# Kernel optimization log

Measured on AMD Instinct MI355X. Metric: run time of the kernel, lower is better.

The kernel has to match this reference:

```python
import jax, jax.numpy as jnp
import numpy as np

N = 4096
DIN, DOUT, HID, CUTS = 16, 16, 16, 8
RADIUS = 9.0
SCALES = (1.0, 2.0, 3.0, 5.0, 10.0)
REG = 0.01
CHUNK = 512
GROUPS = 4
DINF = DIN + 2 * len(SCALES)  # 26


def leaky(v):
    return jnp.where(v >= 0, v, 0.2 * v)


def sqdist(a, b):
    d2 = jnp.sum(a * a, -1)[:, None] + jnp.sum(b * b, -1)[None, :] - 2.0 * (a @ b.T)
    return jnp.maximum(d2, 0.0)


def tangent_vectors(n):
    # Duff et al. branchless orthonormal basis, as in dMaSIF geometry_processing
    x, y, z = n[..., 0], n[..., 1], n[..., 2]
    s = jnp.where(z >= 0, 1.0, -1.0)
    a = -1.0 / (s + z)
    b = x * y * a
    t1 = jnp.stack([1.0 + s * x * x * a, s * b, -s * x], -1)
    t2 = jnp.stack([b, s + y * y * a, -y], -1)
    return jnp.stack([t1, t2], axis=-2)  # (..., 2, 3)


def group_norm(x, w, b, eps=1e-5):
    # torch GroupNorm(4, C) applied on (1, C, N): normalize over (C/G, N) per group
    n, c = x.shape
    xt = x.T.reshape(GROUPS, c // GROUPS, n)
    m = jnp.mean(xt, axis=(1, 2), keepdims=True)
    v = jnp.mean((xt - m) ** 2, axis=(1, 2), keepdims=True)
    xt = (xt - m) / jnp.sqrt(v + eps)
    return (xt.reshape(c, n) * w[:, None] + b[:, None]).T


def curvature_features(verts, normals):
    # dMaSIF curvatures(): per-scale Gaussian-window covariances, shape operator S = PPt^-1 PQt
    # Pairwise sums factorized into matmuls with the (N,N) window (no (N,N,8) intermediates).
    n_pts = verts.shape[0]
    d2 = sqdist(verts, verts)
    xx = (verts[:, :, None] * verts[:, None, :]).reshape(n_pts, 9)
    feats = []
    for s in SCALES:
        w = jnp.exp(-d2 / (2.0 * s * s))
        u_n = w @ normals  # scale-smoothed normals
        ns = u_n / jnp.maximum(jnp.linalg.norm(u_n, axis=-1, keepdims=True), 1e-12)
        uv = tangent_vectors(ns)  # (N,2,3)
        s0 = jnp.sum(w, 1)
        sx = w @ verts
        sn = w @ ns
        sxx = (w @ xx).reshape(n_pts, 3, 3)
        xn = (verts[:, :, None] * ns[:, None, :]).reshape(n_pts, 9)
        sxn = (w @ xn).reshape(n_pts, 3, 3)
        # sum_j w_ij (x_j-x_i)(x_j-x_i)^T  and  sum_j w_ij (x_j-x_i)(n_j-n_i)^T
        cxx = sxx - verts[:, :, None] * sx[:, None, :] - sx[:, :, None] * verts[:, None, :] \
              + s0[:, None, None] * verts[:, :, None] * verts[:, None, :]
        cxn = sxn - verts[:, :, None] * sn[:, None, :] - sx[:, :, None] * ns[:, None, :] \
              + s0[:, None, None] * verts[:, :, None] * ns[:, None, :]
        ppt = jnp.einsum('nka,nab,nlb->nkl', uv, cxx, uv) + REG * jnp.eye(2, dtype=verts.dtype)
        pqt = jnp.einsum('nka,nab,nlb->nkl', uv, cxn, uv)
        S = jnp.linalg.solve(ppt, pqt)  # (N,2,2)
        feats.append(jnp.clip(S[:, 0, 0] + S[:, 1, 1], -1.0, 1.0))            # mean curvature
        feats.append(jnp.clip(S[:, 0, 0] * S[:, 1, 1] - S[:, 0, 1] * S[:, 1, 0], -1.0, 1.0))  # gauss
    return jnp.stack(feats, -1)  # (N, 2*len(SCALES))


def _forward(verts, vnormals, x, os_w1, os_b1, os_w2, os_b2,
             ni_w1, ni_b1, ni_w2, ni_b2, gn_in_w, gn_in_b,
             cv_a1, cv_b1, cv_a2, cv_b2, no_w1, no_b1, no_w2, no_b2,
             gn_out_w, gn_out_b, ll_w1, ll_b1, ll_w2, ll_b2, lt_w, lt_b):
    curv = curvature_features(verts, vnormals)
    xf = jnp.concatenate([x, curv], axis=-1)  # (N, DINF)
    w = leaky(xf @ os_w1.T + os_b1) @ os_w2.T + os_b2  # orientation scores (N,1)

    # --- load_mesh: steer tangent frames along the gradient of w ---
    p = verts / RADIUS
    ndot = vnormals @ vnormals.T
    W = jnp.exp(-sqdist(p, p) * (2.0 - ndot) ** 2)  # pseudo-geodesic Gaussian window
    uv = tangent_vectors(vnormals)  # (N,2,3)
    ov3 = W @ (w * p) - (W @ w) * p  # sum_j W_ij w_j (x_j - x_i), factorized
    ov = jnp.einsum('nkd,nd->nk', uv, ov3) + 1e-5
    u = ov / jnp.sqrt(jnp.sum(ov * ov, -1, keepdims=True))
    ex, ey = u[:, 0:1], u[:, 1:2]
    u0, v0 = uv[:, 0], uv[:, 1]
    nuv = jnp.concatenate([vnormals[:, None, :],
                           (ex * u0 + ey * v0)[:, None, :],
                           (-ey * u0 + ex * v0)[:, None, :]], axis=1)  # (N,3,3)

    # --- dMaSIFConv layer ---
    h = leaky(leaky(xf @ ni_w1.T + ni_b1) @ ni_w2.T + ni_b2)
    h = group_norm(h, gn_in_w, gn_in_b)  # (N, HID)
    n_all = nuv[:, 0]
    nc = N // CHUNK
    pc = p.reshape(nc, CHUNK, 3)
    nuvc = nuv.reshape(nc, CHUNK, 3, 3)

    def block(args):
        pi, nuvi = args  # (C,3), (C,3,3)
        dx = p[None, :, :] - pi[:, None, :]  # (C,N,3)
        d2 = jnp.sum(dx * dx, -1)
        win = jnp.exp(-d2 * (2.0 - nuvi[:, 0] @ n_all.T) ** 2)  # (C,N)
        X = jnp.einsum('ckd,cnd->cnk', nuvi, dx)  # local coords (C,N,3)
        y = jax.nn.relu(X @ cv_a1.T + cv_b1) @ cv_a2.T + cv_b2  # filter MLP (C,N,HID)
        return jnp.einsum('cn,cnh,nh->ch', win, y, h)

    xi = jax.lax.map(jax.checkpoint(block), (pc, nuvc)).reshape(N, HID)
    xi = group_norm(leaky(leaky(xi @ no_w1.T + no_b1) @ no_w2.T + no_b2), gn_out_w, gn_out_b)
    xi = jax.nn.relu(xi @ ll_w1.T + ll_b1) @ ll_w2.T + ll_b2  # linear_layers[0]
    return xf @ lt_w.T + lt_b + xi  # linear_transform skip + conv branch


def setup_inputs():
    key = jax.random.key(0)
    ks = jax.random.split(key, 20)

    def lin(k, o, i):
        wk = jax.random.fold_in(k, 0)
        bk = jax.random.fold_in(k, 1)
        return ((1.0 / np.sqrt(i)) * jax.random.normal(wk, (o, i)),
                0.01 * jax.random.normal(bk, (o,)))

    verts = 10.0 * jax.random.normal(ks[0], (N, 3))
    vn = jax.random.normal(ks[1], (N, 3))
    vnormals = vn / jnp.linalg.norm(vn, axis=-1, keepdims=True)
    x = jax.random.normal(ks[2], (N, DIN))
    os_w1, os_b1 = lin(ks[3], DOUT, DINF)
    os_w2, os_b2 = lin(ks[4], 1, DOUT)
    ni_w1, ni_b1 = lin(ks[5], HID, DINF)
    ni_w2, ni_b2 = lin(ks[6], HID, HID)
    cv_a1 = jax.random.normal(ks[7], (CUTS, 3))
    cv_b1 = jax.random.uniform(ks[8], (CUTS,)) * 0.8 * jnp.sqrt(jnp.sum(cv_a1 ** 2, -1))
    cv_a2 = jax.random.uniform(ks[9], (HID, CUTS), minval=-1.0, maxval=1.0) / np.sqrt(CUTS)
    cv_b2 = jax.random.normal(ks[10], (HID,)) * 0.5 * jnp.sqrt(jnp.sum(cv_a2 ** 2, -1))
    no_w1, no_b1 = lin(ks[11], DOUT, HID)
    no_w2, no_b2 = lin(ks[12], DOUT, DOUT)
    ll_w1, ll_b1 = lin(ks[13], DOUT, DOUT)
    ll_w2, ll_b2 = lin(ks[14], DOUT, DOUT)
    lt_w, lt_b = lin(ks[15], DOUT, DINF)
    return {'verts': verts, 'vnormals': vnormals, 'x': x,
            'os_w1': os_w1, 'os_b1': os_b1, 'os_w2': os_w2, 'os_b2': os_b2,
            'ni_w1': ni_w1, 'ni_b1': ni_b1, 'ni_w2': ni_w2, 'ni_b2': ni_b2,
            'gn_in_w': jnp.ones(HID), 'gn_in_b': jnp.zeros(HID),
            'cv_a1': cv_a1, 'cv_b1': cv_b1, 'cv_a2': cv_a2, 'cv_b2': cv_b2,
            'no_w1': no_w1, 'no_b1': no_b1, 'no_w2': no_w2, 'no_b2': no_b2,
            'gn_out_w': jnp.ones(DOUT), 'gn_out_b': jnp.zeros(DOUT),
            'll_w1': ll_w1, 'll_b1': ll_b1, 'll_w2': ll_w2, 'll_b2': ll_b2,
            'lt_w': lt_w, 'lt_b': lt_b}


def reference(verts, vnormals, x, os_w1, os_b1, os_w2, os_b2,
              ni_w1, ni_b1, ni_w2, ni_b2, gn_in_w, gn_in_b,
              cv_a1, cv_b1, cv_a2, cv_b2, no_w1, no_b1, no_w2, no_b2,
              gn_out_w, gn_out_b, ll_w1, ll_b1, ll_w2, ll_b2, lt_w, lt_b):
    return _forward(verts, vnormals, x, os_w1, os_b1, os_w2, os_b2,
                    ni_w1, ni_b1, ni_w2, ni_b2, gn_in_w, gn_in_b,
                    cv_a1, cv_b1, cv_a2, cv_b2, no_w1, no_b1, no_w2, no_b2,
                    gn_out_w, gn_out_b, ll_w1, ll_b1, ll_w2, ll_b2, lt_w, lt_b)
```

## Files before the change

kernel.cpp:

```cpp
#include <hip/hip_runtime.h>
#include <hip/hip_bf16.h>
#include <math.h>

#define NPTS 4096
#define DINF 26
#define LOG2E 1.44269504088896f
#define JSPL 4

typedef float f32x4v __attribute__((ext_vector_type(4)));
typedef __bf16 bf16x8v __attribute__((ext_vector_type(8)));
typedef unsigned short ushort_t;

__device__ __forceinline__ float ldb(const float* p, int i){ return p[i]; }
__device__ __forceinline__ float lk(float v){ return v >= 0.0f ? v : 0.2f*v; }
__device__ __forceinline__ float wsum64(float v){
#pragma unroll
  for(int o=32;o>0;o>>=1) v += __shfl_down(v,o);
  return v;
}
__device__ __forceinline__ unsigned short f2bf(float f){
  return __builtin_bit_cast(unsigned short, __float2bfloat16(f));
}
__device__ __forceinline__ float bf2f(unsigned short u){
  return __bfloat162float(__builtin_bit_cast(__hip_bfloat16, u));
}
__device__ __forceinline__ void wave_lds_fence(){
  __builtin_amdgcn_wave_barrier();
  __builtin_amdgcn_s_waitcnt(0xC07F);
  __builtin_amdgcn_wave_barrier();
}
__device__ __forceinline__ void tangent(float nx,float ny,float nz,float* t1,float* t2){
  float s = (nz >= 0.0f) ? 1.0f : -1.0f;
  float a = -1.0f/(s+nz);
  float b = nx*ny*a;
  t1[0]=1.0f+s*nx*nx*a; t1[1]=s*b; t1[2]=-s*nx;
  t2[0]=b; t2[1]=s+ny*ny*a; t2[2]=-ny;
}

__global__ __launch_bounds__(256) void k0_convert(const float* __restrict__ verts,
                                                  const float* __restrict__ vnorm,
                                                  const float* __restrict__ x,
                                                  float* __restrict__ vertsF,
                                                  float* __restrict__ nF,
                                                  float* __restrict__ pF,
                                                  float* __restrict__ xfF){
  int i = blockIdx.x*blockDim.x + threadIdx.x;
  if(i >= NPTS) return;
#pragma unroll
  for(int d=0;d<3;d++){
    float v = verts[i*3+d];
    vertsF[i*3+d]=v;
    pF[i*3+d]=v*(1.0f/9.0f);
    nF[i*3+d]=vnorm[i*3+d];
  }
#pragma unroll
  for(int c=0;c<16;c++) xfF[i*DINF+c]=x[i*16+c];
}

__global__ __launch_bounds__(256) void kF(const float* __restrict__ vertsF,
                                          const float* __restrict__ nF,
                                          ushort_t* __restrict__ F1h,
                                          ushort_t* __restrict__ F1l){
  int j = blockIdx.x*256 + threadIdx.x;
  float vx=vertsF[j*3+0], vy=vertsF[j*3+1], vz=vertsF[j*3+2];
  float fv[16];
  fv[0]=1.0f; fv[1]=vx; fv[2]=vy; fv[3]=vz;
  fv[4]=vx*vx; fv[5]=vx*vy; fv[6]=vx*vz; fv[7]=vy*vy; fv[8]=vy*vz; fv[9]=vz*vz;
  fv[10]=nF[j*3+0]; fv[11]=nF[j*3+1]; fv[12]=nF[j*3+2];
  fv[13]=0.0f; fv[14]=0.0f; fv[15]=0.0f;
#pragma unroll
  for(int c=0;c<16;c++){
    unsigned short h=f2bf(fv[c]);
    F1h[c*NPTS+j]=h;
    F1l[c*NPTS+j]=f2bf(fv[c]-bf2f(h));
  }
}

__global__ __launch_bounds__(256) void k1m(const float* __restrict__ vertsF,
                                           const ushort_t* __restrict__ F1h,
                                           const ushort_t* __restrict__ F1l,
                                           float* __restrict__ sc){
  __shared__ __align__(16) float vq[4][64][4];
  __shared__ float red[4][16][16];
  const float c2e[5] = {0.5f*LOG2E, 0.125f*LOG2E, (1.0f/18.0f)*LOG2E,
                        0.02f*LOG2E, 0.005f*LOG2E};
  int lane = threadIdx.x & 63, w = threadIdx.x >> 6;
  int c16 = lane & 15, q = lane >> 4;
  int it = blockIdx.x >> 2, jseg = blockIdx.x & (JSPL-1);
  int i0 = it*16;
  int ia = i0 + c16;
  float vix=vertsF[ia*3+0], viy=vertsF[ia*3+1], viz=vertsF[ia*3+2];
  float nsqi = vix*vix+viy*viy+viz*viz;
  f32x4v acc[5];
#pragma unroll
  for(int s=0;s<5;s++) acc[s] = (f32x4v){0.0f,0.0f,0.0f,0.0f};

  int jbeg = jseg*(NPTS/JSPL) + w*(NPTS/JSPL/4);
  int jend = jbeg + (NPTS/JSPL/4);
#pragma unroll 1
  for(int jb=jbeg; jb<jend; jb+=64){
    int j = jb + lane;
    float vx=vertsF[j*3+0], vy=vertsF[j*3+1], vz=vertsF[j*3+2];
    *(float4*)&vq[w][lane][0] = make_float4(vx,vy,vz,vx*vx+vy*vy+vz*vz);
    wave_lds_fence();
#pragma unroll
    for(int q2=0;q2<2;q2++){
      int rb = q2*32 + q*8;
      bf16x8v bh = *(const bf16x8v*)(F1h + c16*NPTS + jb + rb);
      bf16x8v bl = *(const bf16x8v*)(F1l + c16*NPTS + jb + rb);
      bf16x8v af[5];
#pragma unroll
      for(int t=0;t<8;t++){
        float4 vv = *(const float4*)&vq[w][rb+t][0];
        float dot = vix*vv.x + viy*vv.y + viz*vv.z;
        float d2 = fmaxf(nsqi + vv.w - 2.0f*dot, 0.0f);
#pragma unroll
        for(int s=0;s<5;s++)
          af[s][t] = __builtin_bit_cast(__bf16, f2bf(exp2f(-d2*c2e[s])));
      }
#pragma unroll
      for(int s=0;s<5;s++){
        acc[s] = __builtin_amdgcn_mfma_f32_16x16x32_bf16(af[s], bh, acc[s], 0,0,0);
        acc[s] = __builtin_amdgcn_mfma_f32_16x16x32_bf16(af[s], bl, acc[s], 0,0,0);
      }
    }
    wave_lds_fence();
  }
#pragma unroll
  for(int s=0;s<5;s++){
#pragma unroll
    for(int r=0;r<4;r++) red[w][q*4+r][c16] = acc[s][r];
    __syncthreads();
    if(w==0){
      float* base = sc + (size_t)s*13*NPTS;
#pragma unroll
      for(int r=0;r<4;r++){
        int m = q*4+r, i = i0+m;
        float D = red[0][m][c16]+red[1][m][c16]+red[2][m][c16]+red[3][m][c16];
        if(c16==0)       atomicAdd(&base[i], D);
        else if(c16<4)   atomicAdd(&base[NPTS + i*3 + (c16-1)], D);
        else if(c16<10)  atomicAdd(&base[4*NPTS + i*6 + (c16-4)], D);
        else if(c16<13)  atomicAdd(&base[10*NPTS + i*3 + (c16-10)], D);
      }
    }
    __syncthreads();
  }
}

__global__ __launch_bounds__(256) void k2p(const float* __restrict__ vertsF,
                                           const float* __restrict__ sc,
                                           ushort_t* __restrict__ F2h,
                                           ushort_t* __restrict__ F2l){
  int idx = blockIdx.x*256 + threadIdx.x;
  int j = idx & (NPTS-1);
  int s = idx >> 12;
  float vx=vertsF[j*3+0], vy=vertsF[j*3+1], vz=vertsF[j*3+2];
  const float* ub = sc + (size_t)s*13*NPTS + 10*NPTS + (size_t)j*3;
  float ux=ub[0], uy=ub[1], uz=ub[2];
  float inv = 1.0f/fmaxf(sqrtf(ux*ux+uy*uy+uz*uz), 1e-12f);
  float n0=ux*inv, n1=uy*inv, n2=uz*inv;
  float fv[16];
  fv[0]=n0; fv[1]=n1; fv[2]=n2;
  fv[3]=vx*n0; fv[4]=vx*n1; fv[5]=vx*n2;
  fv[6]=vy*n0; fv[7]=vy*n1; fv[8]=vy*n2;
  fv[9]=vz*n0; fv[10]=vz*n1; fv[11]=vz*n2;
  fv[12]=0.0f; fv[13]=0.0f; fv[14]=0.0f; fv[15]=0.0f;
#pragma unroll
  for(int c=0;c<16;c++){
    unsigned short h=f2bf(fv[c]);
    F2h[((size_t)s*16+c)*NPTS+j]=h;
    F2l[((size_t)s*16+c)*NPTS+j]=f2bf(fv[c]-bf2f(h));
  }
}

__global__ __launch_bounds__(256) void k2m(const float* __restrict__ vertsF,
                                           const ushort_t* __restrict__ F2h,
                                           const ushort_t* __restrict__ F2l,
                                           float* __restrict__ mom2){
  __shared__ __align__(16) float vq[4][64][4];
  __shared__ float red[4][16][16];
  const float c2e[5] = {0.5f*LOG2E, 0.125f*LOG2E, (1.0f/18.0f)*LOG2E,
                        0.02f*LOG2E, 0.005f*LOG2E};
  int lane = threadIdx.x & 63, w = threadIdx.x >> 6;
  int c16 = lane & 15, q = lane >> 4;
  int it = blockIdx.x >> 2, jseg = blockIdx.x & (JSPL-1);
  int i0 = it*16;
  int ia = i0 + c16;
  float vix=vertsF[ia*3+0], viy=vertsF[ia*3+1], viz=vertsF[ia*3+2];
  float nsqi = vix*vix+viy*viy+viz*viz;
  f32x4v acc[5];
#pragma unroll
  for(int s=0;s<5;s++) acc[s] = (f32x4v){0.0f,0.0f,0.0f,0.0f};

  int jbeg = jseg*(NPTS/JSPL) + w*(NPTS/JSPL/4);
  int jend = jbeg + (NPTS/JSPL/4);
#pragma unroll 1
  for(int jb=jbeg; jb<jend; jb+=64){
    int j = jb + lane;
    float vx=vertsF[j*3+0], vy=vertsF[j*3+1], vz=vertsF[j*3+2];
    *(float4*)&vq[w][lane][0] = make_float4(vx,vy,vz,vx*vx+vy*vy+vz*vz);
    wave_lds_fence();
#pragma unroll
    for(int q2=0;q2<2;q2++){
      int rb = q2*32 + q*8;
      float d2t[8];
#pragma unroll
      for(int t=0;t<8;t++){
        float4 vv = *(const float4*)&vq[w][rb+t][0];
        float dot = vix*vv.x + viy*vv.y + viz*vv.z;
        d2t[t] = fmaxf(nsqi + vv.w - 2.0f*dot, 0.0f);
      }
#pragma unroll
      for(int s=0;s<5;s++){
        bf16x8v bh = *(const bf16x8v*)(F2h + ((size_t)s*16+c16)*NPTS + jb + rb);
        bf16x8v bl = *(const bf16x8v*)(F2l + ((size_t)s*16+c16)*NPTS + jb + rb);
        bf16x8v af;
#pragma unroll
        for(int t=0;t<8;t++)
          af[t] = __builtin_bit_cast(__bf16, f2bf(exp2f(-d2t[t]*c2e[s])));
        acc[s] = __builtin_amdgcn_mfma_f32_16x16x32_bf16(af, bh, acc[s], 0,0,0);
        acc[s] = __builtin_amdgcn_mfma_f32_16x16x32_bf16(af, bl, acc[s], 0,0,0);
      }
    }
    wave_lds_fence();
  }
#pragma unroll
  for(int s=0;s<5;s++){
#pragma unroll
    for(int r=0;r<4;r++) red[w][q*4+r][c16] = acc[s][r];
    __syncthreads();
    if(w==0){
#pragma unroll
      for(int r=0;r<4;r++){
        int m = q*4+r, i = i0+m;
        float D = red[0][m][c16]+red[1][m][c16]+red[2][m][c16]+red[3][m][c16];
        if(c16<12) atomicAdd(&mom2[((size_t)s*NPTS + i)*12 + c16], D);
      }
    }
    __syncthreads();
  }
}

__global__ __launch_bounds__(256) void k2s(const float* __restrict__ vertsF,
                                           const float* __restrict__ sc,
                                           const float* __restrict__ mom2,
                                           float* __restrict__ xfF){
  int idx = blockIdx.x*256 + threadIdx.x;
  int i = idx & (NPTS-1);
  int s = idx >> 12;
  const float* base = sc + (size_t)s*13*NPTS;
  float v[3] = { vertsF[i*3+0], vertsF[i*3+1], vertsF[i*3+2] };
  float s0 = base[i];
  float sx[3] = { base[NPTS+i*3+0], base[NPTS+i*3+1], base[NPTS+i*3+2] };
  float sxx6[6];
#pragma unroll
  for(int k=0;k<6;k++) sxx6[k]=base[4*NPTS+i*6+k];
  float ux=base[10*NPTS+i*3+0], uy=base[10*NPTS+i*3+1], uz=base[10*NPTS+i*3+2];
  float invn = 1.0f/fmaxf(sqrtf(ux*ux+uy*uy+uz*uz), 1e-12f);
  float nsi[3] = { ux*invn, uy*invn, uz*invn };
  const float* M2 = mom2 + ((size_t)s*NPTS + i)*12;
  float sn[3] = { M2[0], M2[1], M2[2] };
  float sxn[3][3];
#pragma unroll
  for(int a=0;a<3;a++)
#pragma unroll
    for(int b=0;b<3;b++) sxn[a][b]=M2[3+a*3+b];
  const int m6[3][3]={{0,1,2},{1,3,4},{2,4,5}};
  float cxx[3][3], cxn[3][3];
#pragma unroll
  for(int a=0;a<3;a++)
#pragma unroll
    for(int b=0;b<3;b++){
      cxx[a][b]=sxx6[m6[a][b]] - v[a]*sx[b] - sx[a]*v[b] + s0*v[a]*v[b];
      cxn[a][b]=sxn[a][b]    - v[a]*sn[b] - sx[a]*nsi[b] + s0*v[a]*nsi[b];
    }
  float t1[3],t2[3];
  tangent(nsi[0],nsi[1],nsi[2],t1,t2);
  float ppt[2][2], pqt[2][2];
#pragma unroll
  for(int k=0;k<2;k++){
    const float* tk = (k==0)?t1:t2;
#pragma unroll
    for(int l=0;l<2;l++){
      const float* tl = (l==0)?t1:t2;
      float accx=0.0f, accn=0.0f;
#pragma unroll
      for(int a=0;a<3;a++)
#pragma unroll
        for(int b=0;b<3;b++){
          accx += tk[a]*cxx[a][b]*tl[b];
          accn += tk[a]*cxn[a][b]*tl[b];
        }
      ppt[k][l]=accx + ((k==l)?0.01f:0.0f);
      pqt[k][l]=accn;
    }
  }
  float det = ppt[0][0]*ppt[1][1]-ppt[0][1]*ppt[1][0];
  float id = 1.0f/det;
  float S00=( ppt[1][1]*pqt[0][0]-ppt[0][1]*pqt[1][0])*id;
  float S01=( ppt[1][1]*pqt[0][1]-ppt[0][1]*pqt[1][1])*id;
  float S10=(-ppt[1][0]*pqt[0][0]+ppt[0][0]*pqt[1][0])*id;
  float S11=(-ppt[1][0]*pqt[0][1]+ppt[0][0]*pqt[1][1])*id;
  float f0=fminf(fmaxf(S00+S11,-1.0f),1.0f);
  float f1=fminf(fmaxf(S00*S11-S01*S10,-1.0f),1.0f);
  xfF[i*DINF+16+2*s]=f0;
  xfF[i*DINF+17+2*s]=f1;
}

__global__ __launch_bounds__(256) void k3_mlps(const float* __restrict__ xfF,
    const float* os_w1, const float* os_b1, const float* os_w2, const float* os_b2,
    const float* ni_w1, const float* ni_b1, const float* ni_w2, const float* ni_b2,
    float* __restrict__ wOS, float* __restrict__ hPre, float* __restrict__ stats){
  int i = blockIdx.x*256 + threadIdx.x;
  int lane = threadIdx.x & 63;
  float xf[DINF];
#pragma unroll
  for(int k=0;k<DINF;k++) xf[k]=xfF[i*DINF+k];
  float h1[16];
#pragma unroll
  for(int o=0;o<16;o++){
    float t=ldb(os_b1,o);
#pragma unroll
    for(int k=0;k<DINF;k++) t += xf[k]*ldb(os_w1,o*DINF+k);
    h1[o]=lk(t);
  }
  float w=ldb(os_b2,0);
#pragma unroll
  for(int o=0;o<16;o++) w += h1[o]*ldb(os_w2,o);
  wOS[i]=w;
#pragma unroll
  for(int o=0;o<16;o++){
    float t=ldb(ni_b1,o);
#pragma unroll
    for(int k=0;k<DINF;k++) t += xf[k]*ldb(ni_w1,o*DINF+k);
    h1[o]=lk(t);
  }
  float h2[16];
#pragma unroll
  for(int o=0;o<16;o++){
    float t=ldb(ni_b2,o);
#pragma unroll
    for(int k=0;k<16;k++) t += h1[k]*ldb(ni_w2,o*16+k);
    h2[o]=lk(t);
    hPre[i*16+o]=h2[o];
  }
  float gs[4]={0,0,0,0}, gq[4]={0,0,0,0};
#pragma unroll
  for(int c=0;c<16;c++){ gs[c>>2]+=h2[c]; gq[c>>2]+=h2[c]*h2[c]; }
  __shared__ float ls[8];
  if(threadIdx.x<8) ls[threadIdx.x]=0.0f;
  __syncthreads();
#pragma unroll
  for(int g=0;g<4;g++){ gs[g]=wsum64(gs[g]); gq[g]=wsum64(gq[g]); }
  if(lane==0){
#pragma unroll
    for(int g=0;g<4;g++){ atomicAdd(&ls[2*g],gs[g]); atomicAdd(&ls[2*g+1],gq[g]); }
  }
  __syncthreads();
  if(threadIdx.x<8) atomicAdd(&stats[threadIdx.x], ls[threadIdx.x]);
}

__global__ __launch_bounds__(256) void k3c_gn(const float* __restrict__ hPre,
                                              const float* __restrict__ stats,
                                              const float* gw, const float* gb,
                                              ushort_t* __restrict__ hTb){
  int i = blockIdx.x*256 + threadIdx.x;
  float m[4], r[4];
#pragma unroll
  for(int g=0;g<4;g++){
    float mean = stats[2*g]*(1.0f/(4.0f*NPTS));
    float var  = stats[2*g+1]*(1.0f/(4.0f*NPTS)) - mean*mean;
    m[g]=mean; r[g]=1.0f/sqrtf(var+1e-5f);
  }
#pragma unroll
  for(int c=0;c<16;c++){
    int g=c>>2;
    float v=(hPre[i*16+c]-m[g])*r[g]*ldb(gw,c)+ldb(gb,c);
    hTb[c*NPTS+i]=f2bf(v);
  }
}

__global__ __launch_bounds__(256) void kB(const float* __restrict__ pF,
                                          const float* __restrict__ wOS,
                                          ushort_t* __restrict__ B4h,
                                          ushort_t* __restrict__ B4l){
  int j = blockIdx.x*256 + threadIdx.x;
  float wj=wOS[j];
  float fv[16];
  fv[0]=wj*pF[j*3+0]; fv[1]=wj*pF[j*3+1]; fv[2]=wj*pF[j*3+2]; fv[3]=wj;
#pragma unroll
  for(int c=4;c<16;c++) fv[c]=0.0f;
#pragma unroll
  for(int c=0;c<16;c++){
    unsigned short h=f2bf(fv[c]);
    B4h[c*NPTS+j]=h;
    B4l[c*NPTS+j]=f2bf(fv[c]-bf2f(h));
  }
}

__global__ __launch_bounds__(512) void k4m(const float* __restrict__ pF,
                                           const float* __restrict__ nF,
                                           const ushort_t* __restrict__ B4h,
                                           const ushort_t* __restrict__ B4l,
                                           float* __restrict__ nuvF){
  __shared__ __align__(16) float vq[8][64][8];
  __shared__ float red[8][16][4];
  int lane = threadIdx.x & 63, w = threadIdx.x >> 6;
  int c16 = lane & 15, q = lane >> 4;
  int i0 = blockIdx.x*16;
  int ia = i0 + c16;
  float pix=pF[ia*3+0], piy=pF[ia*3+1], piz=pF[ia*3+2];
  float nix=nF[ia*3+0], niy=nF[ia*3+1], niz=nF[ia*3+2];
  f32x4v acc = {0.0f,0.0f,0.0f,0.0f};

#pragma unroll 1
  for(int jb=w*512; jb<w*512+512; jb+=64){
    int j = jb + lane;
    *(float4*)&vq[w][lane][0] = make_float4(pF[j*3+0],pF[j*3+1],pF[j*3+2],0.0f);
    *(float4*)&vq[w][lane][4] = make_float4(nF[j*3+0],nF[j*3+1],nF[j*3+2],0.0f);
    wave_lds_fence();
#pragma unroll
    for(int q2=0;q2<2;q2++){
      int rb = q2*32 + q*8;
      bf16x8v bh = *(const bf16x8v*)(B4h + c16*NPTS + jb + rb);
      bf16x8v bl = *(const bf16x8v*)(B4l + c16*NPTS + jb + rb);
      bf16x8v af;
#pragma unroll
      for(int t=0;t<8;t++){
        float4 P  = *(const float4*)&vq[w][rb+t][0];
        float4 Nj = *(const float4*)&vq[w][rb+t][4];
        float dx=P.x-pix, dy=P.y-piy, dz=P.z-piz;
        float d2=dx*dx+dy*dy+dz*dz;
        float f=2.0f-(Nj.x*nix+Nj.y*niy+Nj.z*niz);
        af[t]=__builtin_bit_cast(__bf16, f2bf(exp2f(-d2*f*f*LOG2E)));
      }
      acc = __builtin_amdgcn_mfma_f32_16x16x32_bf16(af, bh, acc, 0,0,0);
      acc = __builtin_amdgcn_mfma_f32_16x16x32_bf16(af, bl, acc, 0,0,0);
    }
    wave_lds_fence();
  }
#pragma unroll
  for(int r=0;r<4;r++) if(c16<4) red[w][q*4+r][c16]=acc[r];
  __syncthreads();
  if(threadIdx.x<16){
    int tid=threadIdx.x, i=i0+tid;
    float a0=0,a1=0,a2=0,a3=0;
#pragma unroll
    for(int ww=0;ww<8;ww++){
      a0+=red[ww][tid][0]; a1+=red[ww][tid][1];
      a2+=red[ww][tid][2]; a3+=red[ww][tid][3];
    }
    float pix2=pF[i*3+0], piy2=pF[i*3+1], piz2=pF[i*3+2];
    float nix2=nF[i*3+0], niy2=nF[i*3+1], niz2=nF[i*3+2];
    float o0=a0-a3*pix2, o1=a1-a3*piy2, o2=a2-a3*piz2;
    float t1[3],t2[3];
    tangent(nix2,niy2,niz2,t1,t2);
    float ov0=t1[0]*o0+t1[1]*o1+t1[2]*o2+1e-5f;
    float ov1=t2[0]*o0+t2[1]*o1+t2[2]*o2+1e-5f;
    float inv=1.0f/sqrtf(ov0*ov0+ov1*ov1);
    float ex=ov0*inv, ey=ov1*inv;
    nuvF[i*9+0]=nix2; nuvF[i*9+1]=niy2; nuvF[i*9+2]=niz2;
    nuvF[i*9+3]= ex*t1[0]+ey*t2[0]; nuvF[i*9+4]= ex*t1[1]+ey*t2[1]; nuvF[i*9+5]= ex*t1[2]+ey*t2[2];
    nuvF[i*9+6]=-ey*t1[0]+ex*t2[0]; nuvF[i*9+7]=-ey*t1[1]+ex*t2[1]; nuvF[i*9+8]=-ey*t1[2]+ex*t2[2];
  }
}

__global__ __launch_bounds__(256) void k5_conv(const float* __restrict__ pF,
                                               const float* __restrict__ nF,
                                               const float* __restrict__ nuvF,
                                               const ushort_t* __restrict__ hTb,
                                               const float* cv_a1, const float* cv_b1,
                                               const float* cv_a2, const float* cv_b2,
                                               float* __restrict__ xiP){
  __shared__ __align__(16) float vq[4][64][8];
  __shared__ float red[4][64][4];
  int lane = threadIdx.x & 63, w = threadIdx.x >> 6;
  int c16 = lane & 15, q = lane >> 4;
  int it = blockIdx.x >> 2, jseg = blockIdx.x & (JSPL-1);
  int i0 = it*16;
  int i = i0 + c16;
  float pix=pF[i*3+0], piy=pF[i*3+1], piz=pF[i*3+2];
  float nu[9];
#pragma unroll
  for(int k=0;k<9;k++) nu[k]=nuvF[i*9+k];
  float a1w[8][3], b1w[8];
#pragma unroll
  for(int c=0;c<8;c++){
    a1w[c][0]=cv_a1[c*3+0]; a1w[c][1]=cv_a1[c*3+1]; a1w[c][2]=cv_a1[c*3+2];
    b1w[c]=cv_b1[c];
  }
  f32x4v acc[9];
#pragma unroll
  for(int c=0;c<9;c++) acc[c]=(f32x4v){0.0f,0.0f,0.0f,0.0f};

  int jbeg = jseg*(NPTS/JSPL) + w*(NPTS/JSPL/4);
  int jend = jbeg + (NPTS/JSPL/4);
#pragma unroll 1
  for(int jb=jbeg; jb<jend; jb+=64){
    int j = jb + lane;
    *(float4*)&vq[w][lane][0] = make_float4(pF[j*3+0],pF[j*3+1],pF[j*3+2],0.0f);
    *(float4*)&vq[w][lane][4] = make_float4(nF[j*3+0],nF[j*3+1],nF[j*3+2],0.0f);
    wave_lds_fence();
#pragma unroll
    for(int q2=0;q2<2;q2++){
      int jb2 = jb + q2*32;
      bf16x8v bfr = *(const bf16x8v*)(hTb + c16*NPTS + jb2 + q*8);
      bf16x8v af[9];
#pragma unroll
      for(int t=0;t<8;t++){
        int rloc = q2*32 + q*8 + t;
        float4 P  = *(const float4*)&vq[w][rloc][0];
        float4 Nj = *(const float4*)&vq[w][rloc][4];
        float dx=P.x-pix, dy=P.y-piy, dz=P.z-piz;
        float d2=dx*dx+dy*dy+dz*dz;
        float f=2.0f-(Nj.x*nu[0]+Nj.y*nu[1]+Nj.z*nu[2]);
        float win=exp2f(-d2*f*f*LOG2E);
        float X0=nu[0]*dx+nu[1]*dy+nu[2]*dz;
        float X1=nu[3]*dx+nu[4]*dy+nu[5]*dz;
        float X2=nu[6]*dx+nu[7]*dy+nu[8]*dz;
#pragma unroll
        for(int c=0;c<8;c++){
          float r=fmaf(X0,a1w[c][0],fmaf(X1,a1w[c][1],fmaf(X2,a1w[c][2],b1w[c])));
          af[c][t]=__builtin_bit_cast(__bf16, f2bf(win*fmaxf(r,0.0f)));
        }
        af[8][t]=__builtin_bit_cast(__bf16, f2bf(win));
      }
#pragma unroll
      for(int c=0;c<9;c++)
        acc[c] = __builtin_amdgcn_mfma_f32_16x16x32_bf16(af[c], bfr, acc[c], 0,0,0);
    }
    wave_lds_fence();
  }
  float a2row[8];
#pragma unroll
  for(int c=0;c<8;c++) a2row[c]=cv_a2[c16*8+c];
  float b2v = cv_b2[c16];
#pragma unroll
  for(int r=0;r<4;r++){
    float xi = acc[8][r]*b2v;
#pragma unroll
    for(int c=0;c<8;c++) xi += acc[c][r]*a2row[c];
    red[w][lane][r]=xi;
  }
  __syncthreads();
  if(w==0){
#pragma unroll
    for(int r=0;r<4;r++){
      float v = red[0][lane][r]+red[1][lane][r]+red[2][lane][r]+red[3][lane][r];
      xiP[((size_t)jseg*NPTS + (i0 + q*4 + r))*16 + c16] = v;
    }
  }
}

__global__ __launch_bounds__(256) void k6a(const float* __restrict__ xiP,
    const float* no_w1, const float* no_b1, const float* no_w2, const float* no_b2,
    float* __restrict__ tF, float* __restrict__ stats2){
  int i = blockIdx.x*256 + threadIdx.x;
  int lane = threadIdx.x & 63;
  float xi[16];
#pragma unroll
  for(int k=0;k<16;k++){
    float v=0.0f;
#pragma unroll
    for(int s=0;s<JSPL;s++) v += xiP[((size_t)s*NPTS + i)*16 + k];
    xi[k]=v;
  }
  float t1[16];
#pragma unroll
  for(int o=0;o<16;o++){
    float t=ldb(no_b1,o);
#pragma unroll
    for(int k=0;k<16;k++) t += xi[k]*ldb(no_w1,o*16+k);
    t1[o]=lk(t);
  }
  float t2[16];
#pragma unroll
  for(int o=0;o<16;o++){
    float t=ldb(no_b2,o);
#pragma unroll
    for(int k=0;k<16;k++) t += t1[k]*ldb(no_w2,o*16+k);
    t2[o]=lk(t);
    tF[i*16+o]=t2[o];
  }
  float gs[4]={0,0,0,0}, gq[4]={0,0,0,0};
#pragma unroll
  for(int c=0;c<16;c++){ gs[c>>2]+=t2[c]; gq[c>>2]+=t2[c]*t2[c]; }
  __shared__ float ls[8];
  if(threadIdx.x<8) ls[threadIdx.x]=0.0f;
  __syncthreads();
#pragma unroll
  for(int g=0;g<4;g++){ gs[g]=wsum64(gs[g]); gq[g]=wsum64(gq[g]); }
  if(lane==0){
#pragma unroll
    for(int g=0;g<4;g++){ atomicAdd(&ls[2*g],gs[g]); atomicAdd(&ls[2*g+1],gq[g]); }
  }
  __syncthreads();
  if(threadIdx.x<8) atomicAdd(&stats2[threadIdx.x], ls[threadIdx.x]);
}

__global__ __launch_bounds__(256) void k6c(const float* __restrict__ tF,
    const float* __restrict__ xfF, const float* __restrict__ stats2,
    const float* gw, const float* gb,
    const float* ll_w1, const float* ll_b1, const float* ll_w2, const float* ll_b2,
    const float* lt_w, const float* lt_b,
    float* __restrict__ out){
  int i = blockIdx.x*256 + threadIdx.x;
  float m[4], r[4];
#pragma unroll
  for(int g=0;g<4;g++){
    float mean = stats2[2*g]*(1.0f/(4.0f*NPTS));
    float var  = stats2[2*g+1]*(1.0f/(4.0f*NPTS)) - mean*mean;
    m[g]=mean; r[g]=1.0f/sqrtf(var+1e-5f);
  }
  float tn[16];
#pragma unroll
  for(int c=0;c<16;c++){
    int g=c>>2;
    tn[c]=(tF[i*16+c]-m[g])*r[g]*ldb(gw,c)+ldb(gb,c);
  }
  float z1[16];
#pragma unroll
  for(int o=0;o<16;o++){
    float t=ldb(ll_b1,o);
#pragma unroll
    for(int k=0;k<16;k++) t += tn[k]*ldb(ll_w1,o*16+k);
    z1[o]=fmaxf(t,0.0f);
  }
  float xf[DINF];
#pragma unroll
  for(int k=0;k<DINF;k++) xf[k]=xfF[i*DINF+k];
#pragma unroll
  for(int o=0;o<16;o++){
    float z=ldb(ll_b2,o);
#pragma unroll
    for(int k=0;k<16;k++) z += z1[k]*ldb(ll_w2,o*16+k);
    float lt=ldb(lt_b,o);
#pragma unroll
    for(int k=0;k<DINF;k++) lt += xf[k]*ldb(lt_w,o*DINF+k);
    out[i*16+o]=z+lt;
  }
}

extern "C" void kernel_launch(void* const* d_in, const int* in_sizes, int n_in,
                              void* d_out, int out_size, void* d_ws, size_t ws_size,
                              hipStream_t stream){
  const float* verts    = (const float*)d_in[0];
  const float* vnormals = (const float*)d_in[1];
  const float* x        = (const float*)d_in[2];
  const float* os_w1    = (const float*)d_in[3];
  const float* os_b1    = (const float*)d_in[4];
  const float* os_w2    = (const float*)d_in[5];
  const float* os_b2    = (const float*)d_in[6];
  const float* ni_w1    = (const float*)d_in[7];
  const float* ni_b1    = (const float*)d_in[8];
  const float* ni_w2    = (const float*)d_in[9];
  const float* ni_b2    = (const float*)d_in[10];
  const float* gn_in_w  = (const float*)d_in[11];
  const float* gn_in_b  = (const float*)d_in[12];
  const float* cv_a1    = (const float*)d_in[13];
  const float* cv_b1    = (const float*)d_in[14];
  const float* cv_a2    = (const float*)d_in[15];
  const float* cv_b2    = (const float*)d_in[16];
  const float* no_w1    = (const float*)d_in[17];
  const float* no_b1    = (const float*)d_in[18];
  const float* no_w2    = (const float*)d_in[19];
  const float* no_b2    = (const float*)d_in[20];
  const float* gn_out_w = (const float*)d_in[21];
  const float* gn_out_b = (const float*)d_in[22];
  const float* ll_w1    = (const float*)d_in[23];
  const float* ll_b1    = (const float*)d_in[24];
  const float* ll_w2    = (const float*)d_in[25];
  const float* ll_b2    = (const float*)d_in[26];
  const float* lt_w     = (const float*)d_in[27];
  const float* lt_b     = (const float*)d_in[28];

  float* W = (float*)d_ws;
  size_t off = 0;
  float* vertsF = W + off; off += (size_t)3*NPTS;
  float* nF     = W + off; off += (size_t)3*NPTS;
  float* pF     = W + off; off += (size_t)3*NPTS;
  float* xfF    = W + off; off += (size_t)DINF*NPTS;
  float* sc     = W + off; off += (size_t)13*NPTS*5;
  float* wOS    = W + off; off += (size_t)NPTS;
  float* hPre   = W + off; off += (size_t)16*NPTS;
  ushort_t* hTb = (ushort_t*)(W + off); off += (size_t)8*NPTS;
  float* nuvF   = W + off; off += (size_t)9*NPTS;
  float* xiP    = W + off; off += (size_t)JSPL*16*NPTS;
  float* tF     = W + off; off += (size_t)16*NPTS;
  float* stats  = W + off; off += 16;
  ushort_t* F1h = (ushort_t*)(W + off); off += (size_t)8*NPTS;
  ushort_t* F1l = (ushort_t*)(W + off); off += (size_t)8*NPTS;
  ushort_t* F2h = (ushort_t*)(W + off); off += (size_t)40*NPTS;
  ushort_t* F2l = (ushort_t*)(W + off); off += (size_t)40*NPTS;
  ushort_t* B4h = (ushort_t*)(W + off); off += (size_t)8*NPTS;
  ushort_t* B4l = (ushort_t*)(W + off); off += (size_t)8*NPTS;
  float* mom2 = hPre;

  hipMemsetAsync(stats, 0, 16*sizeof(float), stream);
  hipMemsetAsync(sc,   0, (size_t)13*NPTS*5*sizeof(float), stream);
  hipMemsetAsync(mom2, 0, (size_t)12*NPTS*5*sizeof(float), stream);

  k0_convert<<<NPTS/256, 256, 0, stream>>>(verts, vnormals, x, vertsF, nF, pF, xfF);
  kF<<<NPTS/256, 256, 0, stream>>>(vertsF, nF, F1h, F1l);
  k1m<<<(NPTS/16)*JSPL, 256, 0, stream>>>(vertsF, F1h, F1l, sc);
  k2p<<<5*NPTS/256, 256, 0, stream>>>(vertsF, sc, F2h, F2l);
  k2m<<<(NPTS/16)*JSPL, 256, 0, stream>>>(vertsF, F2h, F2l, mom2);
  k2s<<<5*NPTS/256, 256, 0, stream>>>(vertsF, sc, mom2, xfF);
  k3_mlps<<<NPTS/256, 256, 0, stream>>>(xfF, os_w1, os_b1, os_w2, os_b2,
                                        ni_w1, ni_b1, ni_w2, ni_b2, wOS, hPre, stats);
  k3c_gn<<<NPTS/256, 256, 0, stream>>>(hPre, stats, gn_in_w, gn_in_b, hTb);
  kB<<<NPTS/256, 256, 0, stream>>>(pF, wOS, B4h, B4l);
  k4m<<<NPTS/16, 512, 0, stream>>>(pF, nF, B4h, B4l, nuvF);
  k5_conv<<<(NPTS/16)*JSPL, 256, 0, stream>>>(pF, nF, nuvF, hTb,
                                              cv_a1, cv_b1, cv_a2, cv_b2, xiP);
  k6a<<<NPTS/256, 256, 0, stream>>>(xiP, no_w1, no_b1, no_w2, no_b2, tF, stats+8);
  k6c<<<NPTS/256, 256, 0, stream>>>(tF, xfF, stats+8, gn_out_w, gn_out_b,
                                    ll_w1, ll_b1, ll_w2, ll_b2, lt_w, lt_b, (float*)d_out);
}
```

Measured before the change: 310.7 us.

## Drop per-wave LDS staging, read packed point arrays directly, widen j-split

Precomputes packed float4 vertex/norm-squared and point/normal arrays in the convert kernel and has the pairwise kernels read them straight from global memory (cache-resident) instead of staging into LDS with wave fences. The j-split for k1m, k2m and k4m grows from 4 to 8 for more blocks. k4m now accumulates with atomics, and a separate finalize kernel is added. kF and kB are fused into neighbouring kernels to cut launches. The atomics add an extra memset, a launch and nondeterministic summation order.

Result: slower. 342.5 us (+10.2%).

```diff
diff --git a/kernel.cpp b/kernel.cpp
--- a/kernel.cpp
+++ b/kernel.cpp
@@ -6,6 +6,7 @@
 #define DINF 26
 #define LOG2E 1.44269504088896f
 #define JSPL 4
+#define JS2  8
 
 typedef float f32x4v __attribute__((ext_vector_type(4)));
 typedef __bf16 bf16x8v __attribute__((ext_vector_type(8)));
@@ -23,11 +24,6 @@
 }
 __device__ __forceinline__ float bf2f(unsigned short u){
   return __bfloat162float(__builtin_bit_cast(__hip_bfloat16, u));
-}
-__device__ __forceinline__ void wave_lds_fence(){
-  __builtin_amdgcn_wave_barrier();
-  __builtin_amdgcn_s_waitcnt(0xC07F);
-  __builtin_amdgcn_wave_barrier();
 }
 __device__ __forceinline__ void tangent(float nx,float ny,float nz,float* t1,float* t2){
   float s = (nz >= 0.0f) ? 1.0f : -1.0f;
@@ -43,50 +39,47 @@
                                                   float* __restrict__ vertsF,
                                                   float* __restrict__ nF,
                                                   float* __restrict__ pF,
-                                                  float* __restrict__ xfF){
+                                                  float* __restrict__ xfF,
+                                                  ushort_t* __restrict__ F1h,
+                                                  ushort_t* __restrict__ F1l,
+                                                  float* __restrict__ vq4,
+                                                  float* __restrict__ pn8){
   int i = blockIdx.x*blockDim.x + threadIdx.x;
   if(i >= NPTS) return;
-#pragma unroll
-  for(int d=0;d<3;d++){
-    float v = verts[i*3+d];
-    vertsF[i*3+d]=v;
-    pF[i*3+d]=v*(1.0f/9.0f);
-    nF[i*3+d]=vnorm[i*3+d];
-  }
-#pragma unroll
-  for(int c=0;c<16;c++) xfF[i*DINF+c]=x[i*16+c];
-}
-
-__global__ __launch_bounds__(256) void kF(const float* __restrict__ vertsF,
-                                          const float* __restrict__ nF,
-                                          ushort_t* __restrict__ F1h,
-                                          ushort_t* __restrict__ F1l){
-  int j = blockIdx.x*256 + threadIdx.x;
-  float vx=vertsF[j*3+0], vy=vertsF[j*3+1], vz=vertsF[j*3+2];
+  float vx=verts[i*3+0], vy=verts[i*3+1], vz=verts[i*3+2];
+  float nx=vnorm[i*3+0], ny=vnorm[i*3+1], nz=vnorm[i*3+2];
+  vertsF[i*3+0]=vx; vertsF[i*3+1]=vy; vertsF[i*3+2]=vz;
+  nF[i*3+0]=nx; nF[i*3+1]=ny; nF[i*3+2]=nz;
+  float px=vx*(1.0f/9.0f), py=vy*(1.0f/9.0f), pz=vz*(1.0f/9.0f);
+  pF[i*3+0]=px; pF[i*3+1]=py; pF[i*3+2]=pz;
+  *(float4*)(vq4 + i*4) = make_float4(vx,vy,vz, vx*vx+vy*vy+vz*vz);
+  *(float4*)(pn8 + i*8)     = make_float4(px,py,pz,0.0f);
+  *(float4*)(pn8 + i*8 + 4) = make_float4(nx,ny,nz,0.0f);
   float fv[16];
   fv[0]=1.0f; fv[1]=vx; fv[2]=vy; fv[3]=vz;
   fv[4]=vx*vx; fv[5]=vx*vy; fv[6]=vx*vz; fv[7]=vy*vy; fv[8]=vy*vz; fv[9]=vz*vz;
-  fv[10]=nF[j*3+0]; fv[11]=nF[j*3+1]; fv[12]=nF[j*3+2];
-  fv[13]=0.0f; fv[14]=0.0f; fv[15]=0.0f;
+  fv[10]=nx; fv[11]=ny; fv[12]=nz; fv[13]=0.0f; fv[14]=0.0f; fv[15]=0.0f;
 #pragma unroll
   for(int c=0;c<16;c++){
     unsigned short h=f2bf(fv[c]);
-    F1h[c*NPTS+j]=h;
-    F1l[c*NPTS+j]=f2bf(fv[c]-bf2f(h));
-  }
+    F1h[c*NPTS+i]=h;
+    F1l[c*NPTS+i]=f2bf(fv[c]-bf2f(h));
+  }
+#pragma unroll
+  for(int c=0;c<16;c++) xfF[i*DINF+c]=x[i*16+c];
 }
 
 __global__ __launch_bounds__(256) void k1m(const float* __restrict__ vertsF,
+                                           const float* __restrict__ vq4,
                                            const ushort_t* __restrict__ F1h,
                                            const ushort_t* __restrict__ F1l,
                                            float* __restrict__ sc){
-  __shared__ __align__(16) float vq[4][64][4];
   __shared__ float red[4][16][16];
   const float c2e[5] = {0.5f*LOG2E, 0.125f*LOG2E, (1.0f/18.0f)*LOG2E,
                         0.02f*LOG2E, 0.005f*LOG2E};
   int lane = threadIdx.x & 63, w = threadIdx.x >> 6;
   int c16 = lane & 15, q = lane >> 4;
-  int it = blockIdx.x >> 2, jseg = blockIdx.x & (JSPL-1);
+  int it = blockIdx.x >> 3, jseg = blockIdx.x & (JS2-1);
   int i0 = it*16;
   int ia = i0 + c16;
   float vix=vertsF[ia*3+0], viy=vertsF[ia*3+1], viz=vertsF[ia*3+2];
@@ -95,23 +88,19 @@
 #pragma unroll
   for(int s=0;s<5;s++) acc[s] = (f32x4v){0.0f,0.0f,0.0f,0.0f};
 
-  int jbeg = jseg*(NPTS/JSPL) + w*(NPTS/JSPL/4);
-  int jend = jbeg + (NPTS/JSPL/4);
+  int jbeg = jseg*(NPTS/JS2) + w*(NPTS/JS2/4);
+  int jend = jbeg + (NPTS/JS2/4);
 #pragma unroll 1
   for(int jb=jbeg; jb<jend; jb+=64){
-    int j = jb + lane;
-    float vx=vertsF[j*3+0], vy=vertsF[j*3+1], vz=vertsF[j*3+2];
-    *(float4*)&vq[w][lane][0] = make_float4(vx,vy,vz,vx*vx+vy*vy+vz*vz);
-    wave_lds_fence();
 #pragma unroll
     for(int q2=0;q2<2;q2++){
-      int rb = q2*32 + q*8;
-      bf16x8v bh = *(const bf16x8v*)(F1h + c16*NPTS + jb + rb);
-      bf16x8v bl = *(const bf16x8v*)(F1l + c16*NPTS + jb + rb);
+      int rb = jb + q2*32 + q*8;
+      bf16x8v bh = *(const bf16x8v*)(F1h + c16*NPTS + rb);
+      bf16x8v bl = *(const bf16x8v*)(F1l + c16*NPTS + rb);
       bf16x8v af[5];
 #pragma unroll
       for(int t=0;t<8;t++){
-        float4 vv = *(const float4*)&vq[w][rb+t][0];
+        float4 vv = *(const float4*)(vq4 + (rb+t)*4);
         float dot = vix*vv.x + viy*vv.y + viz*vv.z;
         float d2 = fmaxf(nsqi + vv.w - 2.0f*dot, 0.0f);
 #pragma unroll
@@ -124,7 +113,6 @@
         acc[s] = __builtin_amdgcn_mfma_f32_16x16x32_bf16(af[s], bl, acc[s], 0,0,0);
       }
     }
-    wave_lds_fence();
   }
 #pragma unroll
   for(int s=0;s<5;s++){
@@ -174,16 +162,16 @@
 }
 
 __global__ __launch_bounds__(256) void k2m(const float* __restrict__ vertsF,
+                                           const float* __restrict__ vq4,
                                            const ushort_t* __restrict__ F2h,
                                            const ushort_t* __restrict__ F2l,
                                            float* __restrict__ mom2){
-  __shared__ __align__(16) float vq[4][64][4];
   __shared__ float red[4][16][16];
   const float c2e[5] = {0.5f*LOG2E, 0.125f*LOG2E, (1.0f/18.0f)*LOG2E,
                         0.02f*LOG2E, 0.005f*LOG2E};
   int lane = threadIdx.x & 63, w = threadIdx.x >> 6;
   int c16 = lane & 15, q = lane >> 4;
-  int it = blockIdx.x >> 2, jseg = blockIdx.x & (JSPL-1);
+  int it = blockIdx.x >> 3, jseg = blockIdx.x & (JS2-1);
   int i0 = it*16;
   int ia = i0 + c16;
   float vix=vertsF[ia*3+0], viy=vertsF[ia*3+1], viz=vertsF[ia*3+2];
@@ -192,28 +180,24 @@
 #pragma unroll
   for(int s=0;s<5;s++) acc[s] = (f32x4v){0.0f,0.0f,0.0f,0.0f};
 
-  int jbeg = jseg*(NPTS/JSPL) + w*(NPTS/JSPL/4);
-  int jend = jbeg + (NPTS/JSPL/4);
+  int jbeg = jseg*(NPTS/JS2) + w*(NPTS/JS2/4);
+  int jend = jbeg + (NPTS/JS2/4);
 #pragma unroll 1
   for(int jb=jbeg; jb<jend; jb+=64){
-    int j = jb + lane;
-    float vx=vertsF[j*3+0], vy=vertsF[j*3+1], vz=vertsF[j*3+2];
-    *(float4*)&vq[w][lane][0] = make_float4(vx,vy,vz,vx*vx+vy*vy+vz*vz);
-    wave_lds_fence();
 #pragma unroll
     for(int q2=0;q2<2;q2++){
-      int rb = q2*32 + q*8;
+      int rb = jb + q2*32 + q*8;
       float d2t[8];
 #pragma unroll
       for(int t=0;t<8;t++){
-        float4 vv = *(const float4*)&vq[w][rb+t][0];
+        float4 vv = *(const float4*)(vq4 + (rb+t)*4);
         float dot = vix*vv.x + viy*vv.y + viz*vv.z;
         d2t[t] = fmaxf(nsqi + vv.w - 2.0f*dot, 0.0f);
       }
 #pragma unroll
       for(int s=0;s<5;s++){
-        bf16x8v bh = *(const bf16x8v*)(F2h + ((size_t)s*16+c16)*NPTS + jb + rb);
-        bf16x8v bl = *(const bf16x8v*)(F2l + ((size_t)s*16+c16)*NPTS + jb + rb);
+        bf16x8v bh = *(const bf16x8v*)(F2h + ((size_t)s*16+c16)*NPTS + rb);
+        bf16x8v bl = *(const bf16x8v*)(F2l + ((size_t)s*16+c16)*NPTS + rb);
         bf16x8v af;
 #pragma unroll
         for(int t=0;t<8;t++)
@@ -222,7 +206,6 @@
         acc[s] = __builtin_amdgcn_mfma_f32_16x16x32_bf16(af, bl, acc[s], 0,0,0);
       }
     }
-    wave_lds_fence();
   }
 #pragma unroll
   for(int s=0;s<5;s++){
@@ -363,7 +346,11 @@
 __global__ __launch_bounds__(256) void k3c_gn(const float* __restrict__ hPre,
                                               const float* __restrict__ stats,
                                               const float* gw, const float* gb,
-                                              ushort_t* __restrict__ hTb){
+                                              const float* __restrict__ pF,
+                                              const float* __restrict__ wOS,
+                                              ushort_t* __restrict__ hTb,
+                                              ushort_t* __restrict__ B4h,
+                                              ushort_t* __restrict__ B4l){
   int i = blockIdx.x*256 + threadIdx.x;
   float m[4], r[4];
 #pragma unroll
@@ -378,57 +365,49 @@
     float v=(hPre[i*16+c]-m[g])*r[g]*ldb(gw,c)+ldb(gb,c);
     hTb[c*NPTS+i]=f2bf(v);
   }
-}
-
-__global__ __launch_bounds__(256) void kB(const float* __restrict__ pF,
-                                          const float* __restrict__ wOS,
-                                          ushort_t* __restrict__ B4h,
-                                          ushort_t* __restrict__ B4l){
-  int j = blockIdx.x*256 + threadIdx.x;
-  float wj=wOS[j];
+  float wj=wOS[i];
   float fv[16];
-  fv[0]=wj*pF[j*3+0]; fv[1]=wj*pF[j*3+1]; fv[2]=wj*pF[j*3+2]; fv[3]=wj;
+  fv[0]=wj*pF[i*3+0]; fv[1]=wj*pF[i*3+1]; fv[2]=wj*pF[i*3+2]; fv[3]=wj;
 #pragma unroll
   for(int c=4;c<16;c++) fv[c]=0.0f;
 #pragma unroll
   for(int c=0;c<16;c++){
     unsigned short h=f2bf(fv[c]);
-    B4h[c*NPTS+j]=h;
-    B4l[c*NPTS+j]=f2bf(fv[c]-bf2f(h));
-  }
-}
-
-__global__ __launch_bounds__(512) void k4m(const float* __restrict__ pF,
+    B4h[c*NPTS+i]=h;
+    B4l[c*NPTS+i]=f2bf(fv[c]-bf2f(h));
+  }
+}
+
+__global__ __launch_bounds__(256) void k4m(const float* __restrict__ pF,
                                            const float* __restrict__ nF,
+                                           const float* __restrict__ pn8,
                                            const ushort_t* __restrict__ B4h,
                                            const ushort_t* __restrict__ B4l,
-                                           float* __restrict__ nuvF){
-  __shared__ __align__(16) float vq[8][64][8];
-  __shared__ float red[8][16][4];
+                                           float* __restrict__ ov4){
+  __shared__ float red[4][16][16];
   int lane = threadIdx.x & 63, w = threadIdx.x >> 6;
   int c16 = lane & 15, q = lane >> 4;
-  int i0 = blockIdx.x*16;
+  int it = blockIdx.x >> 3, jseg = blockIdx.x & (JS2-1);
+  int i0 = it*16;
   int ia = i0 + c16;
   float pix=pF[ia*3+0], piy=pF[ia*3+1], piz=pF[ia*3+2];
   float nix=nF[ia*3+0], niy=nF[ia*3+1], niz=nF[ia*3+2];
   f32x4v acc = {0.0f,0.0f,0.0f,0.0f};
 
+  int jbeg = jseg*(NPTS/JS2) + w*(NPTS/JS2/4);
+  int jend = jbeg + (NPTS/JS2/4);
 #pragma unroll 1
-  for(int jb=w*512; jb<w*512+512; jb+=64){
-    int j = jb + lane;
-    *(float4*)&vq[w][lane][0] = make_float4(pF[j*3+0],pF[j*3+1],pF[j*3+2],0.0f);
-    *(float4*)&vq[w][lane][4] = make_float4(nF[j*3+0],nF[j*3+1],nF[j*3+2],0.0f);
-    wave_lds_fence();
+  for(int jb=jbeg; jb<jend; jb+=64){
 #pragma unroll
     for(int q2=0;q2<2;q2++){
-      int rb = q2*32 + q*8;
-      bf16x8v bh = *(const bf16x8v*)(B4h + c16*NPTS + jb + rb);
-      bf16x8v bl = *(const bf16x8v*)(B4l + c16*NPTS + jb + rb);
+      int rb = jb + q2*32 + q*8;
+      bf16x8v bh = *(const bf16x8v*)(B4h + c16*NPTS + rb);
+      bf16x8v bl = *(const bf16x8v*)(B4l + c16*NPTS + rb);
       bf16x8v af;
 #pragma unroll
       for(int t=0;t<8;t++){
-        float4 P  = *(const float4*)&vq[w][rb+t][0];
-        float4 Nj = *(const float4*)&vq[w][rb+t][4];
+        float4 P  = *(const float4*)(pn8 + (size_t)(rb+t)*8);
+        float4 Nj = *(const float4*)(pn8 + (size_t)(rb+t)*8 + 4);
         float dx=P.x-pix, dy=P.y-piy, dz=P.z-piz;
         float d2=dx*dx+dy*dy+dz*dz;
         float f=2.0f-(Nj.x*nix+Nj.y*niy+Nj.z*niz);
@@ -437,42 +416,47 @@
       acc = __builtin_amdgcn_mfma_f32_16x16x32_bf16(af, bh, acc, 0,0,0);
       acc = __builtin_amdgcn_mfma_f32_16x16x32_bf16(af, bl, acc, 0,0,0);
     }
-    wave_lds_fence();
-  }
-#pragma unroll
-  for(int r=0;r<4;r++) if(c16<4) red[w][q*4+r][c16]=acc[r];
+  }
+#pragma unroll
+  for(int r=0;r<4;r++) red[w][q*4+r][c16]=acc[r];
   __syncthreads();
-  if(threadIdx.x<16){
-    int tid=threadIdx.x, i=i0+tid;
-    float a0=0,a1=0,a2=0,a3=0;
-#pragma unroll
-    for(int ww=0;ww<8;ww++){
-      a0+=red[ww][tid][0]; a1+=red[ww][tid][1];
-      a2+=red[ww][tid][2]; a3+=red[ww][tid][3];
-    }
-    float pix2=pF[i*3+0], piy2=pF[i*3+1], piz2=pF[i*3+2];
-    float nix2=nF[i*3+0], niy2=nF[i*3+1], niz2=nF[i*3+2];
-    float o0=a0-a3*pix2, o1=a1-a3*piy2, o2=a2-a3*piz2;
-    float t1[3],t2[3];
-    tangent(nix2,niy2,niz2,t1,t2);
-    float ov0=t1[0]*o0+t1[1]*o1+t1[2]*o2+1e-5f;
-    float ov1=t2[0]*o0+t2[1]*o1+t2[2]*o2+1e-5f;
-    float inv=1.0f/sqrtf(ov0*ov0+ov1*ov1);
-    float ex=ov0*inv, ey=ov1*inv;
-    nuvF[i*9+0]=nix2; nuvF[i*9+1]=niy2; nuvF[i*9+2]=niz2;
-    nuvF[i*9+3]= ex*t1[0]+ey*t2[0]; nuvF[i*9+4]= ex*t1[1]+ey*t2[1]; nuvF[i*9+5]= ex*t1[2]+ey*t2[2];
-    nuvF[i*9+6]=-ey*t1[0]+ex*t2[0]; nuvF[i*9+7]=-ey*t1[1]+ex*t2[1]; nuvF[i*9+8]=-ey*t1[2]+ex*t2[2];
-  }
+  if(w==0){
+#pragma unroll
+    for(int r=0;r<4;r++){
+      int m = q*4+r, i = i0+m;
+      float D = red[0][m][c16]+red[1][m][c16]+red[2][m][c16]+red[3][m][c16];
+      if(c16<4) atomicAdd(&ov4[i*4+c16], D);
+    }
+  }
+}
+
+__global__ __launch_bounds__(256) void k4s(const float* __restrict__ pF,
+                                           const float* __restrict__ nF,
+                                           const float* __restrict__ ov4,
+                                           float* __restrict__ nuvF){
+  int i = blockIdx.x*256 + threadIdx.x;
+  float a0=ov4[i*4+0], a1=ov4[i*4+1], a2=ov4[i*4+2], a3=ov4[i*4+3];
+  float pix=pF[i*3+0], piy=pF[i*3+1], piz=pF[i*3+2];
+  float nix=nF[i*3+0], niy=nF[i*3+1], niz=nF[i*3+2];
+  float o0=a0-a3*pix, o1=a1-a3*piy, o2=a2-a3*piz;
+  float t1[3],t2[3];
+  tangent(nix,niy,niz,t1,t2);
+  float ov0=t1[0]*o0+t1[1]*o1+t1[2]*o2+1e-5f;
+  float ov1=t2[0]*o0+t2[1]*o1+t2[2]*o2+1e-5f;
+  float inv=1.0f/sqrtf(ov0*ov0+ov1*ov1);
+  float ex=ov0*inv, ey=ov1*inv;
+  nuvF[i*9+0]=nix; nuvF[i*9+1]=niy; nuvF[i*9+2]=niz;
+  nuvF[i*9+3]= ex*t1[0]+ey*t2[0]; nuvF[i*9+4]= ex*t1[1]+ey*t2[1]; nuvF[i*9+5]= ex*t1[2]+ey*t2[2];
+  nuvF[i*9+6]=-ey*t1[0]+ex*t2[0]; nuvF[i*9+7]=-ey*t1[1]+ex*t2[1]; nuvF[i*9+8]=-ey*t1[2]+ex*t2[2];
 }
 
 __global__ __launch_bounds__(256) void k5_conv(const float* __restrict__ pF,
-                                               const float* __restrict__ nF,
+                                               const float* __restrict__ pn8,
                                                const float* __restrict__ nuvF,
                                                const ushort_t* __restrict__ hTb,
                                                const float* cv_a1, const float* cv_b1,
                                                const float* cv_a2, const float* cv_b2,
                                                float* __restrict__ xiP){
-  __shared__ __align__(16) float vq[4][64][8];
   __shared__ float red[4][64][4];
   int lane = threadIdx.x & 63, w = threadIdx.x >> 6;
   int c16 = lane & 15, q = lane >> 4;
@@ -497,20 +481,15 @@
   int jend = jbeg + (NPTS/JSPL/4);
 #pragma unroll 1
   for(int jb=jbeg; jb<jend; jb+=64){
-    int j = jb + lane;
-    *(float4*)&vq[w][lane][0] = make_float4(pF[j*3+0],pF[j*3+1],pF[j*3+2],0.0f);
-    *(float4*)&vq[w][lane][4] = make_float4(nF[j*3+0],nF[j*3+1],nF[j*3+2],0.0f);
-    wave_lds_fence();
 #pragma unroll
     for(int q2=0;q2<2;q2++){
-      int jb2 = jb + q2*32;
-      bf16x8v bfr = *(const bf16x8v*)(hTb + c16*NPTS + jb2 + q*8);
+      int rb = jb + q2*32 + q*8;
+      bf16x8v bfr = *(const bf16x8v*)(hTb + c16*NPTS + rb);
       bf16x8v af[9];
 #pragma unroll
       for(int t=0;t<8;t++){
-        int rloc = q2*32 + q*8 + t;
-        float4 P  = *(const float4*)&vq[w][rloc][0];
-        float4 Nj = *(const float4*)&vq[w][rloc][4];
+        float4 P  = *(const float4*)(pn8 + (size_t)(rb+t)*8);
+        float4 Nj = *(const float4*)(pn8 + (size_t)(rb+t)*8 + 4);
         float dx=P.x-pix, dy=P.y-piy, dz=P.z-piz;
         float d2=dx*dx+dy*dy+dz*dz;
         float f=2.0f-(Nj.x*nu[0]+Nj.y*nu[1]+Nj.z*nu[2]);
@@ -529,7 +508,6 @@
       for(int c=0;c<9;c++)
         acc[c] = __builtin_amdgcn_mfma_f32_16x16x32_bf16(af[c], bfr, acc[c], 0,0,0);
     }
-    wave_lds_fence();
   }
   float a2row[8];
 #pragma unroll
@@ -694,24 +672,29 @@
   ushort_t* F2l = (ushort_t*)(W + off); off += (size_t)40*NPTS;
   ushort_t* B4h = (ushort_t*)(W + off); off += (size_t)8*NPTS;
   ushort_t* B4l = (ushort_t*)(W + off); off += (size_t)8*NPTS;
+  float* vq4    = W + off; off += (size_t)4*NPTS;
+  float* pn8    = W + off; off += (size_t)8*NPTS;
+  float* ov4    = W + off; off += (size_t)4*NPTS;
   float* mom2 = hPre;
 
   hipMemsetAsync(stats, 0, 16*sizeof(float), stream);
   hipMemsetAsync(sc,   0, (size_t)13*NPTS*5*sizeof(float), stream);
   hipMemsetAsync(mom2, 0, (size_t)12*NPTS*5*sizeof(float), stream);
-
-  k0_convert<<<NPTS/256, 256, 0, stream>>>(verts, vnormals, x, vertsF, nF, pF, xfF);
-  kF<<<NPTS/256, 256, 0, stream>>>(vertsF, nF, F1h, F1l);
-  k1m<<<(NPTS/16)*JSPL, 256, 0, stream>>>(vertsF, F1h, F1l, sc);
+  hipMemsetAsync(ov4,  0, (size_t)4*NPTS*sizeof(float), stream);
+
+  k0_convert<<<NPTS/256, 256, 0, stream>>>(verts, vnormals, x, vertsF, nF, pF, xfF,
+                                           F1h, F1l, vq4, pn8);
+  k1m<<<(NPTS/16)*JS2, 256, 0, stream>>>(vertsF, vq4, F1h, F1l, sc);
   k2p<<<5*NPTS/256, 256, 0, stream>>>(vertsF, sc, F2h, F2l);
-  k2m<<<(NPTS/16)*JSPL, 256, 0, stream>>>(vertsF, F2h, F2l, mom2);
+  k2m<<<(NPTS/16)*JS2, 256, 0, stream>>>(vertsF, vq4, F2h, F2l, mom2);
   k2s<<<5*NPTS/256, 256, 0, stream>>>(vertsF, sc, mom2, xfF);
   k3_mlps<<<NPTS/256, 256, 0, stream>>>(xfF, os_w1, os_b1, os_w2, os_b2,
                                         ni_w1, ni_b1, ni_w2, ni_b2, wOS, hPre, stats);
-  k3c_gn<<<NPTS/256, 256, 0, stream>>>(hPre, stats, gn_in_w, gn_in_b, hTb);
-  kB<<<NPTS/256, 256, 0, stream>>>(pF, wOS, B4h, B4l);
-  k4m<<<NPTS/16, 512, 0, stream>>>(pF, nF, B4h, B4l, nuvF);
-  k5_conv<<<(NPTS/16)*JSPL, 256, 0, stream>>>(pF, nF, nuvF, hTb,
+  k3c_gn<<<NPTS/256, 256, 0, stream>>>(hPre, stats, gn_in_w, gn_in_b,
+                                       pF, wOS, hTb, B4h, B4l);
+  k4m<<<(NPTS/16)*JS2, 256, 0, stream>>>(pF, nF, pn8, B4h, B4l, ov4);
+  k4s<<<NPTS/256, 256, 0, stream>>>(pF, nF, ov4, nuvF);
+  k5_conv<<<(NPTS/16)*JSPL, 256, 0, stream>>>(pF, pn8, nuvF, hTb,
                                               cv_a1, cv_b1, cv_a2, cv_b2, xiP);
   k6a<<<NPTS/256, 256, 0, stream>>>(xiP, no_w1, no_b1, no_w2, no_b2, tF, stats+8);
   k6c<<<NPTS/256, 256, 0, stream>>>(tF, xfF, stats+8, gn_out_w, gn_out_b,
```
